# Performance work log

Measured on AMD Instinct MI355X. Metric: run time of the kernel, lower is better.

Reference implementation:

```python
import jax, jax.numpy as jnp
import numpy as np
import math

B, LL, LP = 16, 256, 1024
HID, H = 128, 8
SCALE = math.sqrt(HID)


def setup_inputs() -> dict:
    key = jax.random.key(0)
    ks = jax.random.split(key, 20)
    s = 0.02
    inp = {
        "ligand": jax.random.normal(ks[0], (B, LL, HID), jnp.float32),
        "prot": jax.random.normal(ks[1], (B, LP, HID), jnp.float32),
        "inter": jax.random.uniform(ks[2], (B, 1, LL, LP), jnp.float32),
        # projection weights stored as [in, out] (x @ W + b)
        "Wl1": jax.random.normal(ks[3], (HID, HID * H), jnp.float32) * s,
        "bl1": jnp.zeros((HID * H,), jnp.float32),
        "Wl2": jax.random.normal(ks[4], (HID, HID * H), jnp.float32) * s,
        "bl2": jnp.zeros((HID * H,), jnp.float32),
        "Wp1": jax.random.normal(ks[5], (HID, HID * H), jnp.float32) * s,
        "bp1": jnp.zeros((HID * H,), jnp.float32),
        "Wp2": jax.random.normal(ks[6], (HID, HID * H), jnp.float32) * s,
        "bp2": jnp.zeros((HID * H,), jnp.float32),
        "W11": jax.random.normal(ks[7], (HID * H, HID), jnp.float32) * s,
        "b11": jnp.zeros((HID,), jnp.float32),
        "W12": jax.random.normal(ks[8], (2 * HID, HID), jnp.float32) * s,
        "b12": jnp.zeros((HID,), jnp.float32),
        "W21": jax.random.normal(ks[9], (HID * H, HID), jnp.float32) * s,
        "b21": jnp.zeros((HID,), jnp.float32),
        "W22": jax.random.normal(ks[10], (2 * HID, HID), jnp.float32) * s,
        "b22": jnp.zeros((HID,), jnp.float32),
    }
    return inp


def _heads(x):
    # [B, L, H*D] -> [B, H, L, D]
    b, l, _ = x.shape
    return x.reshape(b, l, H, HID).transpose(0, 2, 1, 3)


def reference(ligand, prot, inter, Wl1, bl1, Wl2, bl2, Wp1, bp1, Wp2, bp2,
              W11, b11, W12, b12, W21, b21, W22, b22):
    relu = jax.nn.relu
    l1 = _heads(relu(ligand @ Wl1 + bl1))   # [B,H,LL,D]
    l2 = _heads(relu(ligand @ Wl2 + bl2))   # [B,H,LL,D]
    p1 = _heads(relu(prot @ Wp1 + bp1))     # [B,H,LP,D]
    p2 = _heads(relu(prot @ Wp2 + bp2))     # [B,H,LP,D]

    energy = jnp.einsum('bhld,bhpd->bhlp', l1, p1) / SCALE
    att = jax.nn.softmax(energy * inter, axis=-1)  # dropout is identity at eval

    # ligand branch: att @ prot2 -> [B,LL,H*D]
    lig3 = jnp.einsum('bhlp,bhpd->blhd', att, p2).reshape(B, LL, H * HID)
    lig3 = jnp.concatenate([lig3 @ W11 + b11, ligand], axis=2)
    lig3 = relu(lig3 @ W12 + b12)

    # protein branch: att^T @ ligand2 -> [B,LP,H*D]
    prot3 = jnp.einsum('bhlp,bhld->bphd', att, l2).reshape(B, LP, H * HID)
    prot3 = jnp.concatenate([prot3 @ W21 + b21, prot], axis=2)
    prot3 = relu(prot3 @ W22 + b22)
    return (lig3, prot3)
```

## Files before the change

### kernel.cpp

```cpp
#include <hip/hip_runtime.h>
#include <hip/hip_bf16.h>

typedef unsigned short u16;
typedef __attribute__((ext_vector_type(4))) float f32x4;
typedef __attribute__((ext_vector_type(4))) unsigned int u32x4;
typedef __attribute__((ext_vector_type(4))) unsigned short u16x4;
typedef __attribute__((ext_vector_type(8))) unsigned short u16x8;
typedef __attribute__((ext_vector_type(8))) __bf16 bf16x8;

__device__ inline float u2f(u16 u) {
    union { unsigned int i; float f; } x; x.i = ((unsigned int)u) << 16; return x.f;
}
__device__ inline u16 f2u(float f) {
    __hip_bfloat16 b = __float2bfloat16(f);
    return *reinterpret_cast<u16*>(&b);
}
__device__ inline f32x4 mfma16(bf16x8 a, bf16x8 b, f32x4 c) {
    return __builtin_amdgcn_mfma_f32_16x16x32_bf16(a, b, c, 0, 0, 0);
}
__device__ inline void gload_lds16(const u16* g, u16* l) {
    __builtin_amdgcn_global_load_lds(
        (const __attribute__((address_space(1))) unsigned int*)g,
        (__attribute__((address_space(3))) unsigned int*)l, 16, 0, 0);
}

__global__ __launch_bounds__(256)
void proj_kernel(const u16* __restrict__ ligb, const u16* __restrict__ protb,
                 const u16* __restrict__ Wl1t, const u16* __restrict__ Wl2t,
                 const u16* __restrict__ Wp1t, const u16* __restrict__ Wp2t,
                 const float* __restrict__ bl1, const float* __restrict__ bl2,
                 const float* __restrict__ bp1, const float* __restrict__ bp2,
                 u16* __restrict__ l1v, u16* __restrict__ l2tv,
                 u16* __restrict__ p1v, u16* __restrict__ p2tv)
{
    __shared__ __align__(16) u16 As[128 * 64];
    __shared__ __align__(16) u16 Bs[128 * 64];
    const int y = blockIdx.y;
    const u16* A; const u16* B; const float* bias; u16* Out;
    int mode, logL, my;
    if (y < 32)       { A = ligb;  B = Wl1t; bias = bl1; Out = l1v;  mode = 1; logL = 8;  my = y; }
    else if (y < 64)  { A = ligb;  B = Wl2t; bias = bl2; Out = l2tv; mode = 3; logL = 8;  my = y - 32; }
    else if (y < 192) { A = protb; B = Wp1t; bias = bp1; Out = p1v;  mode = 1; logL = 10; my = y - 64; }
    else              { A = protb; B = Wp2t; bias = bp2; Out = p2tv; mode = 3; logL = 10; my = y - 192; }
    const int n0 = blockIdx.x * 128, m0 = my * 128;
    const int tid = threadIdx.x;
    const int w = tid >> 6, lane = tid & 63, q = lane >> 4, li = lane & 15;
    const int wr = w >> 1, wc = w & 1;

    const int srow = tid >> 3;
    const int cg = (tid & 7) ^ (srow & 7);
    const int ldsbase = ((tid >> 6) * 8) * 64;

    f32x4 acc[4][4];
    #pragma unroll
    for (int i = 0; i < 4; i++)
        #pragma unroll
        for (int j = 0; j < 4; j++) acc[i][j] = (f32x4){0.f, 0.f, 0.f, 0.f};

    #pragma unroll
    for (int kt = 0; kt < 128; kt += 64) {
        const u16* Ab = A + (long)m0 * 128 + kt + cg * 8;
        const u16* Bb = B + (long)n0 * 128 + kt + cg * 8;
        #pragma unroll
        for (int c = 0; c < 4; c++) {
            gload_lds16(Ab + (long)(c * 32 + srow) * 128, &As[ldsbase + c * 32 * 64]);
            gload_lds16(Bb + (long)(c * 32 + srow) * 128, &Bs[ldsbase + c * 32 * 64]);
        }
        __syncthreads();
        #pragma unroll
        for (int s = 0; s < 2; s++) {
            const int cp = ((s * 4 + q) ^ (li & 7)) * 8;
            bf16x8 av[4], bv[4];
            #pragma unroll
            for (int i = 0; i < 4; i++)
                av[i] = *(bf16x8*)&As[(wr * 64 + i * 16 + li) * 64 + cp];
            #pragma unroll
            for (int j = 0; j < 4; j++)
                bv[j] = *(bf16x8*)&Bs[(wc * 64 + j * 16 + li) * 64 + cp];
            #pragma unroll
            for (int i = 0; i < 4; i++)
                #pragma unroll
                for (int j = 0; j < 4; j++)
                    acc[i][j] = mfma16(av[i], bv[j], acc[i][j]);
        }
        __syncthreads();
    }

    const int Lm = (1 << logL) - 1;
    #pragma unroll
    for (int i = 0; i < 4; i++) {
        #pragma unroll
        for (int j = 0; j < 4; j++) {
            const int col = n0 + wc * 64 + j * 16 + li;
            const float bvs = bias[col];
            if (mode == 3) {
                const int row0 = m0 + wr * 64 + i * 16 + q * 4;
                long base = ((long)(((row0 >> logL) * 8 + (col >> 7)) * 128
                            + (col & 127)) << logL) + (row0 & Lm);
                u16x4 o;
                #pragma unroll
                for (int r = 0; r < 4; r++)
                    o[r] = f2u(fmaxf(acc[i][j][r] + bvs, 0.f));
                *(u16x4*)(Out + base) = o;
            } else {
                #pragma unroll
                for (int r = 0; r < 4; r++) {
                    const int row = m0 + wr * 64 + i * 16 + q * 4 + r;
                    long addr = ((long)((row >> logL) * 8 + (col >> 7)) << (logL + 7))
                              + ((long)(row & Lm) << 7) + (col & 127);
                    Out[addr] = f2u(fmaxf(acc[i][j][r] + bvs, 0.f));
                }
            }
        }
    }
}

__global__ __launch_bounds__(512)
void av_kernel(const u16* __restrict__ att, const u16* __restrict__ p2t,
               const u16* __restrict__ l2t,
               u16* __restrict__ lig3, u16* __restrict__ prot3)
{
    __shared__ __align__(16) u16 As[256 * 64];
    __shared__ __align__(16) u16 Bs[128 * 64];
    __shared__ __align__(16) u16 T[64 * 256];
    const int bid = blockIdx.x;
    const int tid = threadIdx.x;
    const int w = tid >> 6, lane = tid & 63, q = lane >> 4, li = lane & 15;
    const int wr = w >> 1, wc = w & 1;

    f32x4 acc[4][4];
    #pragma unroll
    for (int i = 0; i < 4; i++)
        #pragma unroll
        for (int j = 0; j < 4; j++) acc[i][j] = (f32x4){0.f, 0.f, 0.f, 0.f};

    if (bid < 128) {
        const int bh = bid;
        const u16* A = att + (long)bh * 262144;
        const u16* B = p2t + (long)bh * 131072;
        const int srow = tid >> 3;
        const int cg = (tid & 7) ^ (srow & 7);
        const int ldsbase = ((tid >> 6) * 8) * 64;

        for (int kt = 0; kt < 1024; kt += 64) {
            const u16* Ab = A + kt + cg * 8;
            const u16* Bb = B + kt + cg * 8;
            #pragma unroll
            for (int c = 0; c < 4; c++)
                gload_lds16(Ab + (long)(c * 64 + srow) * 1024,
                            &As[ldsbase + c * 64 * 64]);
            #pragma unroll
            for (int c = 0; c < 2; c++)
                gload_lds16(Bb + (long)(c * 64 + srow) * 1024,
                            &Bs[ldsbase + c * 64 * 64]);
            __syncthreads();
            #pragma unroll
            for (int s = 0; s < 2; s++) {
                const int cp = ((s * 4 + q) ^ (li & 7)) * 8;
                bf16x8 av[4], bv[4];
                #pragma unroll
                for (int i = 0; i < 4; i++)
                    av[i] = *(bf16x8*)&As[(wr * 64 + i * 16 + li) * 64 + cp];
                #pragma unroll
                for (int j = 0; j < 4; j++)
                    bv[j] = *(bf16x8*)&Bs[(wc * 64 + j * 16 + li) * 64 + cp];
                #pragma unroll
                for (int i = 0; i < 4; i++)
                    #pragma unroll
                    for (int j = 0; j < 4; j++)
                        acc[i][j] = mfma16(av[i], bv[j], acc[i][j]);
            }
            __syncthreads();
        }

        const long obase = ((long)(bh >> 3) * 256) * 1024 + (long)(bh & 7) * 128;
        #pragma unroll
        for (int i = 0; i < 4; i++)
            #pragma unroll
            for (int j = 0; j < 4; j++) {
                const int col = wc * 64 + j * 16 + li;
                #pragma unroll
                for (int r = 0; r < 4; r++) {
                    const int row = wr * 64 + i * 16 + q * 4 + r;
                    lig3[obase + (long)row * 1024 + col] = f2u(acc[i][j][r]);
                }
            }
    } else {
        const int pb = bid - 128;
        const int bh = pb >> 2;
        const int m0 = (pb & 3) * 256;
        const u16* A = att + (long)bh * 262144;
        const u16* B = l2t + (long)bh * 32768;
        const int w6 = tid >> 6;
        const int i5 = (tid >> 5) & 1;
        const int srow = tid >> 3;
        const int cg = (tid & 7) ^ (srow & 7);
        const int bldsbase = w6 * 8 * 64;

        for (int kt = 0; kt < 256; kt += 64) {
            #pragma unroll
            for (int c = 0; c < 4; c++) {
                gload_lds16(A + (long)(kt + w6 * 8 + c * 2 + i5) * 1024
                              + m0 + (tid & 31) * 8,
                            &T[w6 * 2048 + c * 512]);
            }
            #pragma unroll
            for (int c = 0; c < 2; c++)
                gload_lds16(B + (long)(c * 64 + srow) * 256 + kt + cg * 8,
                            &Bs[bldsbase + c * 64 * 64]);
            __syncthreads();

            #pragma unroll
            for (int pass = 0; pass < 4; pass++) {
                const int p = pass * 64 + (tid & 63);
                union { u16 e[8]; u32x4 v; } tmp;
                #pragma unroll
                for (int e = 0; e < 8; e++)
                    tmp.e[e] = T[(w6 * 8 + e) * 256 + p];
                *(u32x4*)&As[p * 64 + ((w6 ^ (p & 7)) * 8)] = tmp.v;
            }
            __syncthreads();

            #pragma unroll
            for (int s = 0; s < 2; s++) {
                const int cp = ((s * 4 + q) ^ (li & 7)) * 8;
                bf16x8 av[4], bv[4];
                #pragma unroll
                for (int i = 0; i < 4; i++)
                    av[i] = *(bf16x8*)&As[(wr * 64 + i * 16 + li) * 64 + cp];
                #pragma unroll
                for (int j = 0; j < 4; j++)
                    bv[j] = *(bf16x8*)&Bs[(wc * 64 + j * 16 + li) * 64 + cp];
                #pragma unroll
                for (int i = 0; i < 4; i++)
                    #pragma unroll
                    for (int j = 0; j < 4; j++)
                        acc[i][j] = mfma16(av[i], bv[j], acc[i][j]);
            }
            __syncthreads();
        }

        const long obase = ((long)(bh >> 3) * 1024 + m0) * 1024 + (long)(bh & 7) * 128;
        #pragma unroll
        for (int i = 0; i < 4; i++)
            #pragma unroll
            for (int j = 0; j < 4; j++) {
                const int col = wc * 64 + j * 16 + li;
                #pragma unroll
                for (int r = 0; r < 4; r++) {
                    const int row = wr * 64 + i * 16 + q * 4 + r;
                    prot3[obase + (long)row * 1024 + col] = f2u(acc[i][j][r]);
                }
            }
    }
}

__global__ __launch_bounds__(256)
void finals_kernel(const u16* __restrict__ lig3, const u16* __restrict__ ligb,
                   const u16* __restrict__ WstL, const float* __restrict__ bcL,
                   float* __restrict__ out0,
                   const u16* __restrict__ prot3, const u16* __restrict__ protb,
                   const u16* __restrict__ WstP, const float* __restrict__ bcP,
                   float* __restrict__ out1)
{
    __shared__ __align__(16) u16 As[128 * 64];
    __shared__ __align__(16) u16 Bs[128 * 64];
    const int y = blockIdx.y;
    const u16 *A, *A2, *B; const float* bias; float* Out; int my;
    if (y < 32) { A = lig3;  A2 = ligb;  B = WstL; bias = bcL; Out = out0; my = y; }
    else        { A = prot3; A2 = protb; B = WstP; bias = bcP; Out = out1; my = y - 32; }
    const int m0 = my * 128;
    const int tid = threadIdx.x;
    const int w = tid >> 6, lane = tid & 63, q = lane >> 4, li = lane & 15;
    const int wr = w >> 1, wc = w & 1;

    const int srow = tid >> 3;
    const int cg = (tid & 7) ^ (srow & 7);
    const int ldsbase = ((tid >> 6) * 8) * 64;

    f32x4 acc[4][4];
    #pragma unroll
    for (int i = 0; i < 4; i++)
        #pragma unroll
        for (int j = 0; j < 4; j++) acc[i][j] = (f32x4){0.f, 0.f, 0.f, 0.f};

    for (int kt = 0; kt < 1152; kt += 64) {
        const u16* Abase; long lda; int ktA;
        if (kt >= 1024) { Abase = A2; lda = 128; ktA = kt - 1024; }
        else            { Abase = A;  lda = 1024; ktA = kt; }
        const u16* Ab = Abase + (long)m0 * lda + ktA + cg * 8;
        const u16* Bb = B + kt + cg * 8;
        #pragma unroll
        for (int c = 0; c < 4; c++) {
            gload_lds16(Ab + (long)(c * 32 + srow) * lda,  &As[ldsbase + c * 32 * 64]);
            gload_lds16(Bb + (long)(c * 32 + srow) * 1152, &Bs[ldsbase + c * 32 * 64]);
        }
        __syncthreads();
        #pragma unroll
        for (int s = 0; s < 2; s++) {
            const int cp = ((s * 4 + q) ^ (li & 7)) * 8;
            bf16x8 av[4], bv[4];
            #pragma unroll
            for (int i = 0; i < 4; i++)
                av[i] = *(bf16x8*)&As[(wr * 64 + i * 16 + li) * 64 + cp];
            #pragma unroll
            for (int j = 0; j < 4; j++)
                bv[j] = *(bf16x8*)&Bs[(wc * 64 + j * 16 + li) * 64 + cp];
            #pragma unroll
            for (int i = 0; i < 4; i++)
                #pragma unroll
                for (int j = 0; j < 4; j++)
                    acc[i][j] = mfma16(av[i], bv[j], acc[i][j]);
        }
        __syncthreads();
    }

    #pragma unroll
    for (int i = 0; i < 4; i++)
        #pragma unroll
        for (int j = 0; j < 4; j++) {
            const int col = wc * 64 + j * 16 + li;
            const float bvs = bias[col];
            #pragma unroll
            for (int r = 0; r < 4; r++) {
                const int row = m0 + wr * 64 + i * 16 + q * 4 + r;
                Out[(long)row * 128 + col] = fmaxf(acc[i][j][r] + bvs, 0.f);
            }
        }
}

__global__ __launch_bounds__(256, 5)
void attn_kernel(const u16* __restrict__ l1, const u16* __restrict__ p1,
                 const u16* __restrict__ interb, u16* __restrict__ att)
{
    __shared__ __align__(16) u16 S[16 * 1024];
    const int bh = blockIdx.y;
    const int b  = bh >> 3;
    const int m0 = blockIdx.x * 16;
    const int tid = threadIdx.x;
    const float rscale = 0.08838834764831845f;

    {
        const int w = tid >> 6, lane = tid & 63, q = lane >> 4, li = lane & 15;
        bf16x8 af[4];
        const u16* lp = l1 + ((long)bh * 256 + m0 + li) * 128 + q * 8;
        #pragma unroll
        for (int s = 0; s < 4; s++) af[s] = *(const bf16x8*)(lp + s * 32);
        const int sw = q << 4;
        #pragma unroll 4
        for (int t = 0; t < 16; t++) {
            const int n0 = w * 256 + t * 16;
            const u16* bp = p1 + ((long)bh * 1024 + n0 + li) * 128 + q * 8;
            f32x4 acc = (f32x4){0.f, 0.f, 0.f, 0.f};
            #pragma unroll
            for (int s = 0; s < 4; s++)
                acc = mfma16(af[s], *(const bf16x8*)(bp + s * 32), acc);
            #pragma unroll
            for (int r = 0; r < 4; r++) {
                const int row = q * 4 + r;
                S[(row << 10) + ((n0 + li) ^ sw)] = f2u(acc[r] * rscale);
            }
        }
    }
    __syncthreads();

    const int row = tid >> 4;
    const int lj  = tid & 15;
    const int l   = m0 + row;
    const int sw2 = (row >> 2) << 4;
    const u16* ib = interb + ((long)b * 256 + l) * 1024;

    float mx = -1e30f;
    #pragma unroll
    for (int blk = 0; blk < 8; blk++) {
        const int c = blk * 128 + lj * 8;
        u16* sp = &S[(row << 10) + (c ^ sw2)];
        u16x8 s8 = *(u16x8*)sp;
        u16x8 i8 = *(const u16x8*)(ib + c);
        u16x8 o8;
        #pragma unroll
        for (int e = 0; e < 8; e++) {
            float v = u2f(s8[e]) * u2f(i8[e]);
            mx = fmaxf(mx, v);
            o8[e] = f2u(v);
        }
        *(u16x8*)sp = o8;
    }
    #pragma unroll
    for (int d = 1; d < 16; d <<= 1) mx = fmaxf(mx, __shfl_xor(mx, d, 64));

    float z = 0.f;
    #pragma unroll
    for (int blk = 0; blk < 8; blk++) {
        const int c = blk * 128 + lj * 8;
        u16x8 p8 = *(u16x8*)&S[(row << 10) + (c ^ sw2)];
        #pragma unroll
        for (int e = 0; e < 8; e++) z += __expf(u2f(p8[e]) - mx);
    }
    #pragma unroll
    for (int d = 1; d < 16; d <<= 1) z += __shfl_xor(z, d, 64);
    const float inv = 1.f / z;

    u16* op = att + ((long)bh * 256 + l) * 1024;
    #pragma unroll
    for (int blk = 0; blk < 8; blk++) {
        const int c = blk * 128 + lj * 8;
        u16x8 p8 = *(u16x8*)&S[(row << 10) + (c ^ sw2)];
        u16x8 o8;
        #pragma unroll
        for (int e = 0; e < 8; e++)
            o8[e] = f2u(__expf(u2f(p8[e]) - mx) * inv);
        *(u16x8*)(op + c) = o8;
    }
}

struct TPF { const float* src; u16* dst; int R; int C; };
struct TPF8 { TPF t[8]; };

__global__ __launch_bounds__(256)
void cvtw_kernel(TPF8 args)
{
    TPF tp = args.t[blockIdx.z];
    const int c0 = blockIdx.x * 32, r0 = blockIdx.y * 32;
    if (c0 >= tp.C || r0 >= tp.R) return;
    __shared__ u16 tile[32][33];
    const int tx = threadIdx.x & 31, ty = threadIdx.x >> 5;
    #pragma unroll
    for (int i = 0; i < 4; i++)
        tile[ty + i * 8][tx] = f2u(tp.src[(long)(r0 + ty + i * 8) * tp.C + c0 + tx]);
    __syncthreads();
    #pragma unroll
    for (int i = 0; i < 4; i++)
        tp.dst[(long)(c0 + ty + i * 8) * tp.R + r0 + tx] = tile[tx][ty + i * 8];
}

__global__ __launch_bounds__(256)
void wcomb_kernel(const u16* __restrict__ Wm0, const u16* __restrict__ Wo0,
                  const float* __restrict__ bm0, const float* __restrict__ bo0,
                  u16* __restrict__ Wst0, float* __restrict__ bc0,
                  const u16* __restrict__ Wm1, const u16* __restrict__ Wo1,
                  const float* __restrict__ bm1, const float* __restrict__ bo1,
                  u16* __restrict__ Wst1, float* __restrict__ bc1)
{
    const int zz = blockIdx.y;
    const u16* Wm = zz ? Wm1 : Wm0;
    const u16* Wo = zz ? Wo1 : Wo0;
    const float* bmid = zz ? bm1 : bm0;
    const float* bout = zz ? bo1 : bo0;
    u16* Wst = zz ? Wst1 : Wst0;
    float* bc = zz ? bc1 : bc0;
    const int n = blockIdx.x;
    const int tid = threadIdx.x;
    __shared__ float wrow[128];
    if (tid < 128) wrow[tid] = u2f(Wo[n * 256 + tid]);
    __syncthreads();
    for (int k = tid; k < 1024; k += 256) {
        float acc = 0.f;
        #pragma unroll 4
        for (int j = 0; j < 128; j++) acc += wrow[j] * u2f(Wm[(long)j * 1024 + k]);
        Wst[(long)n * 1152 + k] = f2u(acc);
    }
    if (tid < 128) Wst[(long)n * 1152 + 1024 + tid] = Wo[n * 256 + 128 + tid];
    if (tid == 0) {
        float acc = bout[n];
        for (int j = 0; j < 128; j++) acc += bmid[j] * wrow[j];
        bc[n] = acc;
    }
}

__global__ __launch_bounds__(256)
void cvt3_kernel(const float* __restrict__ a, u16* __restrict__ da, int na,
                 const float* __restrict__ b, u16* __restrict__ db, int nb,
                 const float* __restrict__ c, u16* __restrict__ dc, int nc)
{
    const int zz = blockIdx.y;
    const float* s = zz == 0 ? a : (zz == 1 ? b : c);
    u16* d = zz == 0 ? da : (zz == 1 ? db : dc);
    const int n = zz == 0 ? na : (zz == 1 ? nb : nc);
    const int i = (blockIdx.x * 256 + threadIdx.x) * 4;
    if (i >= n) return;
    const float4 v = *(const float4*)(s + i);
    u16x4 o;
    o.x = f2u(v.x); o.y = f2u(v.y); o.z = f2u(v.z); o.w = f2u(v.w);
    *(u16x4*)(d + i) = o;
}

extern "C" void kernel_launch(void* const* d_in, const int* in_sizes, int n_in,
                              void* d_out, int out_size, void* d_ws, size_t ws_size,
                              hipStream_t stream)
{
    (void)in_sizes; (void)n_in; (void)out_size; (void)ws_size;
    const float* ligand = (const float*)d_in[0];
    const float* prot   = (const float*)d_in[1];
    const float* inter  = (const float*)d_in[2];
    const float* Wl1 = (const float*)d_in[3];  const float* bl1 = (const float*)d_in[4];
    const float* Wl2 = (const float*)d_in[5];  const float* bl2 = (const float*)d_in[6];
    const float* Wp1 = (const float*)d_in[7];  const float* bp1 = (const float*)d_in[8];
    const float* Wp2 = (const float*)d_in[9];  const float* bp2 = (const float*)d_in[10];
    const float* W11 = (const float*)d_in[11]; const float* b11 = (const float*)d_in[12];
    const float* W12 = (const float*)d_in[13]; const float* b12 = (const float*)d_in[14];
    const float* W21 = (const float*)d_in[15]; const float* b21 = (const float*)d_in[16];
    const float* W22 = (const float*)d_in[17]; const float* b22 = (const float*)d_in[18];

    float* out0 = (float*)d_out;
    float* out1 = out0 + (size_t)16 * 256 * 128;

    u16* ws = (u16*)d_ws;
    size_t off = 0;
    auto alloc = [&](size_t n) { u16* p = ws + off; off += n; return p; };
    u16* ligb  = alloc(524288);
    u16* protb = alloc(2097152);
    u16* l1v   = alloc(4194304);
    u16* l2t   = alloc(4194304);
    u16* p1v   = alloc(16777216);
    u16* p2t   = alloc(16777216);
    u16* attv  = alloc(33554432);
    u16* lig3  = alloc(4194304);
    u16* prot3 = alloc(16777216);
    u16* Wl1t  = alloc(131072);
    u16* Wl2t  = alloc(131072);
    u16* Wp1t  = alloc(131072);
    u16* Wp2t  = alloc(131072);
    u16* W11t  = alloc(131072);
    u16* W21t  = alloc(131072);
    u16* W12t  = alloc(32768);
    u16* W22t  = alloc(32768);
    u16* WstL  = alloc(147456);
    u16* WstP  = alloc(147456);
    float* bcL = (float*)alloc(256);
    float* bcP = (float*)alloc(256);

    u16* interb = lig3;

    cvt3_kernel<<<dim3(4096, 3), 256, 0, stream>>>(
        ligand, ligb, 524288, prot, protb, 2097152, inter, interb, 4194304);

    TPF8 tp;
    tp.t[0] = {Wl1, Wl1t, 128, 1024};
    tp.t[1] = {Wl2, Wl2t, 128, 1024};
    tp.t[2] = {Wp1, Wp1t, 128, 1024};
    tp.t[3] = {Wp2, Wp2t, 128, 1024};
    tp.t[4] = {W11, W11t, 1024, 128};
    tp.t[5] = {W21, W21t, 1024, 128};
    tp.t[6] = {W12, W12t, 256, 128};
    tp.t[7] = {W22, W22t, 256, 128};
    cvtw_kernel<<<dim3(32, 32, 8), 256, 0, stream>>>(tp);

    wcomb_kernel<<<dim3(128, 2), 256, 0, stream>>>(
        W11t, W12t, b11, b12, WstL, bcL,
        W21t, W22t, b21, b22, WstP, bcP);

    proj_kernel<<<dim3(8, 320), 256, 0, stream>>>(
        ligb, protb, Wl1t, Wl2t, Wp1t, Wp2t,
        bl1, bl2, bp1, bp2, l1v, l2t, p1v, p2t);

    attn_kernel<<<dim3(16, 128), 256, 0, stream>>>(l1v, p1v, interb, attv);

    av_kernel<<<dim3(640), 512, 0, stream>>>(attv, p2t, l2t, lig3, prot3);

    finals_kernel<<<dim3(1, 160), 256, 0, stream>>>(
        lig3, ligb, WstL, bcL, out0,
        prot3, protb, WstP, bcP, out1);
}
```

Measured before the change: 320.1 us.

## Stage P1 tiles through LDS and double attention row tile per block

The attention kernel now handles 32 query rows per 512-thread block instead of 16 per 256-thread block. P1 tiles are staged into swizzled LDS with direct global-to-LDS loads, so all waves share each key tile rather than each wave reading P1 from global memory. Blocks are remapped to a 1D grid that interleaves batch-heads, likely for cache locality. This adds two barriers per key tile and raises LDS use to about 80KB per block, which may reduce occupancy. The softmax phase that follows still indexes rows with tid>>4, which with 512 threads covers 32 rows.

New measurement: 282.5 us. -11.7%, faster.

```diff
diff --git a/kernel.cpp b/kernel.cpp
--- a/kernel.cpp
+++ b/kernel.cpp
@@ -329,40 +329,52 @@
         }
 }
 
-__global__ __launch_bounds__(256, 5)
+__global__ __launch_bounds__(512, 4)
 void attn_kernel(const u16* __restrict__ l1, const u16* __restrict__ p1,
                  const u16* __restrict__ interb, u16* __restrict__ att)
 {
-    __shared__ __align__(16) u16 S[16 * 1024];
-    const int bh = blockIdx.y;
+    __shared__ __align__(16) u16 S[32 * 1024];
+    __shared__ __align__(16) u16 Bs[2][64 * 64];
+    const int id = blockIdx.x;
+    const int bh = (id & 7) * 16 + (id >> 6);
+    const int mt = (id >> 3) & 7;
     const int b  = bh >> 3;
-    const int m0 = blockIdx.x * 16;
+    const int m0 = mt * 32;
     const int tid = threadIdx.x;
     const float rscale = 0.08838834764831845f;
 
     {
         const int w = tid >> 6, lane = tid & 63, q = lane >> 4, li = lane & 15;
+        const int rgrp = w >> 2, pc = w & 3;
+        const int srow = tid >> 3;
+        const int cg = (tid & 7) ^ (srow & 7);
         bf16x8 af[4];
-        const u16* lp = l1 + ((long)bh * 256 + m0 + li) * 128 + q * 8;
+        const u16* lp = l1 + ((long)bh * 256 + m0 + rgrp * 16 + li) * 128 + q * 8;
         #pragma unroll
         for (int s = 0; s < 4; s++) af[s] = *(const bf16x8*)(lp + s * 32);
-        const int sw = q << 4;
-        #pragma unroll 4
-        for (int t = 0; t < 16; t++) {
-            const int n0 = w * 256 + t * 16;
-            const u16* bp = p1 + ((long)bh * 1024 + n0 + li) * 128 + q * 8;
+        const int sw = (rgrp * 4 + q) << 4;
+        const u16* pbase = p1 + ((long)bh * 1024 + srow) * 128 + cg * 8;
+        u16* ldst = &Bs[0][(tid >> 6) * 8 * 64];
+
+        for (int pt = 0; pt < 16; pt++) {
+            gload_lds16(pbase + (long)pt * 8192,      ldst);
+            gload_lds16(pbase + (long)pt * 8192 + 64, ldst + 64 * 64);
+            __syncthreads();
             f32x4 acc = (f32x4){0.f, 0.f, 0.f, 0.f};
             #pragma unroll
-            for (int s = 0; s < 4; s++)
-                acc = mfma16(af[s], *(const bf16x8*)(bp + s * 32), acc);
-            #pragma unroll
-            for (int r = 0; r < 4; r++) {
-                const int row = q * 4 + r;
-                S[(row << 10) + ((n0 + li) ^ sw)] = f2u(acc[r] * rscale);
-            }
-        }
-    }
-    __syncthreads();
+            for (int ks = 0; ks < 4; ks++) {
+                bf16x8 bv = *(bf16x8*)&Bs[ks >> 1][(pc * 16 + li) * 64
+                              + ((((ks & 1) * 4 + q) ^ (li & 7)) * 8)];
+                acc = mfma16(af[ks], bv, acc);
+            }
+            const int col = pt * 64 + pc * 16 + li;
+            const int lr0 = rgrp * 16 + q * 4;
+            #pragma unroll
+            for (int r = 0; r < 4; r++)
+                S[((lr0 + r) << 10) + (col ^ sw)] = f2u(acc[r] * rscale);
+            __syncthreads();
+        }
+    }
 
     const int row = tid >> 4;
     const int lj  = tid & 15;
@@ -554,7 +566,7 @@
         ligb, protb, Wl1t, Wl2t, Wp1t, Wp2t,
         bl1, bl2, bp1, bp2, l1v, l2t, p1v, p2t);
 
-    attn_kernel<<<dim3(16, 128), 256, 0, stream>>>(l1v, p1v, interb, attv);
+    attn_kernel<<<dim3(1024), 512, 0, stream>>>(l1v, p1v, interb, attv);
 
     av_kernel<<<dim3(640), 512, 0, stream>>>(attv, p2t, l2t, lig3, prot3);
 
```

## Remap block indices for XCD locality, widen attn blocks, halve finals tile

Applied to the files above, without the earlier changes.

The attention and AV kernels now decode a flat block id so that blocks sharing the same batch-head land on the same XCD (id & 7), which should improve L2 reuse of att/p1/p2 data. The attention kernel moves to 512 threads with 8 waves each computing 128 columns using prefetched B fragments, and the softmax uses 32 lanes per row. The finals GEMM uses 64-row tiles, doubling the grid to 320 blocks for better CU occupancy at the cost of reloading the weight tile more often.

Measured after the change: 314.5 us. About the same (-1.8%).

```diff
diff --git a/kernel.cpp b/kernel.cpp
--- a/kernel.cpp
+++ b/kernel.cpp
@@ -123,7 +123,10 @@
     __shared__ __align__(16) u16 As[256 * 64];
     __shared__ __align__(16) u16 Bs[128 * 64];
     __shared__ __align__(16) u16 T[64 * 256];
-    const int bid = blockIdx.x;
+    const int id = blockIdx.x;
+    const int slot = id >> 3;
+    const int bh = (id & 7) * 16 + slot / 5;
+    const int role = slot % 5;
     const int tid = threadIdx.x;
     const int w = tid >> 6, lane = tid & 63, q = lane >> 4, li = lane & 15;
     const int wr = w >> 1, wc = w & 1;
@@ -134,8 +137,7 @@
         #pragma unroll
         for (int j = 0; j < 4; j++) acc[i][j] = (f32x4){0.f, 0.f, 0.f, 0.f};
 
-    if (bid < 128) {
-        const int bh = bid;
+    if (role == 0) {
         const u16* A = att + (long)bh * 262144;
         const u16* B = p2t + (long)bh * 131072;
         const int srow = tid >> 3;
@@ -186,9 +188,7 @@
                 }
             }
     } else {
-        const int pb = bid - 128;
-        const int bh = pb >> 2;
-        const int m0 = (pb & 3) * 256;
+        const int m0 = (role - 1) * 256;
         const u16* A = att + (long)bh * 262144;
         const u16* B = l2t + (long)bh * 32768;
         const int w6 = tid >> 6;
@@ -263,13 +263,13 @@
                    const u16* __restrict__ WstP, const float* __restrict__ bcP,
                    float* __restrict__ out1)
 {
-    __shared__ __align__(16) u16 As[128 * 64];
+    __shared__ __align__(16) u16 As[64 * 64];
     __shared__ __align__(16) u16 Bs[128 * 64];
     const int y = blockIdx.y;
     const u16 *A, *A2, *B; const float* bias; float* Out; int my;
-    if (y < 32) { A = lig3;  A2 = ligb;  B = WstL; bias = bcL; Out = out0; my = y; }
-    else        { A = prot3; A2 = protb; B = WstP; bias = bcP; Out = out1; my = y - 32; }
-    const int m0 = my * 128;
+    if (y < 64) { A = lig3;  A2 = ligb;  B = WstL; bias = bcL; Out = out0; my = y; }
+    else        { A = prot3; A2 = protb; B = WstP; bias = bcP; Out = out1; my = y - 64; }
+    const int m0 = my * 64;
     const int tid = threadIdx.x;
     const int w = tid >> 6, lane = tid & 63, q = lane >> 4, li = lane & 15;
     const int wr = w >> 1, wc = w & 1;
@@ -278,9 +278,9 @@
     const int cg = (tid & 7) ^ (srow & 7);
     const int ldsbase = ((tid >> 6) * 8) * 64;
 
-    f32x4 acc[4][4];
-    #pragma unroll
-    for (int i = 0; i < 4; i++)
+    f32x4 acc[2][4];
+    #pragma unroll
+    for (int i = 0; i < 2; i++)
         #pragma unroll
         for (int j = 0; j < 4; j++) acc[i][j] = (f32x4){0.f, 0.f, 0.f, 0.f};
 
@@ -291,23 +291,24 @@
         const u16* Ab = Abase + (long)m0 * lda + ktA + cg * 8;
         const u16* Bb = B + kt + cg * 8;
         #pragma unroll
-        for (int c = 0; c < 4; c++) {
+        for (int c = 0; c < 2; c++)
             gload_lds16(Ab + (long)(c * 32 + srow) * lda,  &As[ldsbase + c * 32 * 64]);
+        #pragma unroll
+        for (int c = 0; c < 4; c++)
             gload_lds16(Bb + (long)(c * 32 + srow) * 1152, &Bs[ldsbase + c * 32 * 64]);
-        }
         __syncthreads();
         #pragma unroll
         for (int s = 0; s < 2; s++) {
             const int cp = ((s * 4 + q) ^ (li & 7)) * 8;
-            bf16x8 av[4], bv[4];
-            #pragma unroll
-            for (int i = 0; i < 4; i++)
-                av[i] = *(bf16x8*)&As[(wr * 64 + i * 16 + li) * 64 + cp];
+            bf16x8 av[2], bv[4];
+            #pragma unroll
+            for (int i = 0; i < 2; i++)
+                av[i] = *(bf16x8*)&As[(wr * 32 + i * 16 + li) * 64 + cp];
             #pragma unroll
             for (int j = 0; j < 4; j++)
                 bv[j] = *(bf16x8*)&Bs[(wc * 64 + j * 16 + li) * 64 + cp];
             #pragma unroll
-            for (int i = 0; i < 4; i++)
+            for (int i = 0; i < 2; i++)
                 #pragma unroll
                 for (int j = 0; j < 4; j++)
                     acc[i][j] = mfma16(av[i], bv[j], acc[i][j]);
@@ -316,27 +317,30 @@
     }
 
     #pragma unroll
-    for (int i = 0; i < 4; i++)
+    for (int i = 0; i < 2; i++)
         #pragma unroll
         for (int j = 0; j < 4; j++) {
             const int col = wc * 64 + j * 16 + li;
             const float bvs = bias[col];
             #pragma unroll
             for (int r = 0; r < 4; r++) {
-                const int row = m0 + wr * 64 + i * 16 + q * 4 + r;
+                const int row = m0 + wr * 32 + i * 16 + q * 4 + r;
                 Out[(long)row * 128 + col] = fmaxf(acc[i][j][r] + bvs, 0.f);
             }
         }
 }
 
-__global__ __launch_bounds__(256, 5)
+__global__ __launch_bounds__(512, 8)
 void attn_kernel(const u16* __restrict__ l1, const u16* __restrict__ p1,
                  const u16* __restrict__ interb, u16* __restrict__ att)
 {
     __shared__ __align__(16) u16 S[16 * 1024];
-    const int bh = blockIdx.y;
+    const int id = blockIdx.x;
+    const int slot = id >> 3;
+    const int bh = (id & 7) * 16 + (slot >> 4);
+    const int mt = slot & 15;
     const int b  = bh >> 3;
-    const int m0 = blockIdx.x * 16;
+    const int m0 = mt * 16;
     const int tid = threadIdx.x;
     const float rscale = 0.08838834764831845f;
 
@@ -346,34 +350,36 @@
         const u16* lp = l1 + ((long)bh * 256 + m0 + li) * 128 + q * 8;
         #pragma unroll
         for (int s = 0; s < 4; s++) af[s] = *(const bf16x8*)(lp + s * 32);
-        const int sw = q << 4;
-        #pragma unroll 4
-        for (int t = 0; t < 16; t++) {
-            const int n0 = w * 256 + t * 16;
-            const u16* bp = p1 + ((long)bh * 1024 + n0 + li) * 128 + q * 8;
+        const u16* bp0 = p1 + ((long)bh * 1024 + w * 128 + li) * 128 + q * 8;
+        #pragma unroll
+        for (int pf = 0; pf < 8; pf++) {
+            const u16* bp = bp0 + (long)pf * 2048;
+            bf16x8 bv[4];
+            #pragma unroll
+            for (int s = 0; s < 4; s++) bv[s] = *(const bf16x8*)(bp + s * 32);
             f32x4 acc = (f32x4){0.f, 0.f, 0.f, 0.f};
             #pragma unroll
-            for (int s = 0; s < 4; s++)
-                acc = mfma16(af[s], *(const bf16x8*)(bp + s * 32), acc);
+            for (int s = 0; s < 4; s++) acc = mfma16(af[s], bv[s], acc);
+            const int col = w * 128 + pf * 16 + li;
             #pragma unroll
             for (int r = 0; r < 4; r++) {
                 const int row = q * 4 + r;
-                S[(row << 10) + ((n0 + li) ^ sw)] = f2u(acc[r] * rscale);
+                S[(row << 10) + (col ^ ((row >> 2) << 4))] = f2u(acc[r] * rscale);
             }
         }
     }
     __syncthreads();
 
-    const int row = tid >> 4;
-    const int lj  = tid & 15;
+    const int row = tid >> 5;
+    const int lj  = tid & 31;
     const int l   = m0 + row;
     const int sw2 = (row >> 2) << 4;
     const u16* ib = interb + ((long)b * 256 + l) * 1024;
 
     float mx = -1e30f;
     #pragma unroll
-    for (int blk = 0; blk < 8; blk++) {
-        const int c = blk * 128 + lj * 8;
+    for (int blk = 0; blk < 4; blk++) {
+        const int c = blk * 256 + lj * 8;
         u16* sp = &S[(row << 10) + (c ^ sw2)];
         u16x8 s8 = *(u16x8*)sp;
         u16x8 i8 = *(const u16x8*)(ib + c);
@@ -387,24 +393,24 @@
         *(u16x8*)sp = o8;
     }
     #pragma unroll
-    for (int d = 1; d < 16; d <<= 1) mx = fmaxf(mx, __shfl_xor(mx, d, 64));
+    for (int d = 1; d < 32; d <<= 1) mx = fmaxf(mx, __shfl_xor(mx, d, 64));
 
     float z = 0.f;
     #pragma unroll
-    for (int blk = 0; blk < 8; blk++) {
-        const int c = blk * 128 + lj * 8;
+    for (int blk = 0; blk < 4; blk++) {
+        const int c = blk * 256 + lj * 8;
         u16x8 p8 = *(u16x8*)&S[(row << 10) + (c ^ sw2)];
         #pragma unroll
         for (int e = 0; e < 8; e++) z += __expf(u2f(p8[e]) - mx);
     }
     #pragma unroll
-    for (int d = 1; d < 16; d <<= 1) z += __shfl_xor(z, d, 64);
+    for (int d = 1; d < 32; d <<= 1) z += __shfl_xor(z, d, 64);
     const float inv = 1.f / z;
 
     u16* op = att + ((long)bh * 256 + l) * 1024;
     #pragma unroll
-    for (int blk = 0; blk < 8; blk++) {
-        const int c = blk * 128 + lj * 8;
+    for (int blk = 0; blk < 4; blk++) {
+        const int c = blk * 256 + lj * 8;
         u16x8 p8 = *(u16x8*)&S[(row << 10) + (c ^ sw2)];
         u16x8 o8;
         #pragma unroll
@@ -554,11 +560,11 @@
         ligb, protb, Wl1t, Wl2t, Wp1t, Wp2t,
         bl1, bl2, bp1, bp2, l1v, l2t, p1v, p2t);
 
-    attn_kernel<<<dim3(16, 128), 256, 0, stream>>>(l1v, p1v, interb, attv);
+    attn_kernel<<<dim3(2048), 512, 0, stream>>>(l1v, p1v, interb, attv);
 
     av_kernel<<<dim3(640), 512, 0, stream>>>(attv, p2t, l2t, lig3, prot3);
 
-    finals_kernel<<<dim3(1, 160), 256, 0, stream>>>(
+    finals_kernel<<<dim3(1, 320), 256, 0, stream>>>(
         lig3, ligb, WstL, bcL, out0,
         prot3, protb, WstP, bcP, out1);
 }
```
